# Optimization experiments

Measured on AMD Instinct MI355X. Metric: run time of the kernel, lower is better.

## Reference

```python
import jax, jax.numpy as jnp
import numpy as np

# Dims: N=batch graphs, V=grid nodes (128x128), D=feature dim, E=edges, L=gnn layers
N, V, D, E, L = 16, 16384, 128, 65536, 2
EPS = 1e-5  # BatchNorm1d default eps


def setup_inputs() -> dict:
    key = jax.random.key(0)
    ks = jax.random.split(key, 8)
    H = jax.random.normal(ks[0], (N, V, D), dtype=jnp.float32)
    edge_src = jax.random.randint(ks[1], (E,), 0, V, dtype=jnp.int32)
    edge_dst = jax.random.randint(ks[2], (E,), 0, V, dtype=jnp.int32)
    A_vals = jax.random.uniform(ks[3], (E,), dtype=jnp.float32)
    scale = 1.0 / np.sqrt(D).astype(np.float32)
    # Stacked per-layer params. Linear stores weight as [out, in]; y = x @ W.T
    W_self = jax.random.normal(ks[4], (L, D, D), dtype=jnp.float32) * scale
    W_nei = jax.random.normal(ks[5], (L, D, D), dtype=jnp.float32) * scale
    gamma = jnp.ones((L, D), dtype=jnp.float32)
    beta = jnp.zeros((L, D), dtype=jnp.float32)
    return {"H": H, "edge_src": edge_src, "edge_dst": edge_dst, "A_vals": A_vals,
            "W_self": W_self, "W_nei": W_nei, "gamma": gamma, "beta": beta}


def reference(H, edge_src, edge_dst, A_vals, W_self, W_nei, gamma, beta):
    X = H  # [N, V, D]
    for l in range(L):
        # SpMM: X_nei[n] = A_norm @ X[n], batched over N via vmap.
        msg = X[:, edge_src, :] * A_vals[None, :, None]  # [N, E, D]
        X_nei = jax.vmap(
            lambda m: jax.ops.segment_sum(m, edge_dst, num_segments=V)
        )(msg)  # [N, V, D]
        # y = x @ W.T for torch Linear(weight=[out,in])
        Y = (jnp.einsum('nvd,ed->nve', X, W_self[l])
             + jnp.einsum('nvd,ed->nve', X_nei, W_nei[l]))  # [N, V, D]
        # BatchNorm1d in training mode over the flattened (N*V) batch dim
        mean = jnp.mean(Y, axis=(0, 1))            # [D]
        var = jnp.var(Y, axis=(0, 1))              # biased variance, [D]
        Y = (Y - mean) * jax.lax.rsqrt(var + EPS) * gamma[l] + beta[l]
        X = jax.nn.relu(Y)
    return X
```

## Files before the change

kernel.cpp:

```cpp
#include <hip/hip_runtime.h>

#define N_ 16
#define V_ 16384
#define D_ 128
#define E_ 65536
#define L_ 2
#define M_ (N_*V_)


typedef __attribute__((ext_vector_type(8))) short short8;
typedef __attribute__((ext_vector_type(4))) float floatx4;

__device__ inline unsigned short f2bf(float x){
  unsigned u = __builtin_bit_cast(unsigned, x);
  unsigned r = u + 0x7fffu + ((u >> 16) & 1u);
  return (unsigned short)(r >> 16);
}
__device__ inline float bf2f(unsigned short h){
  unsigned u = ((unsigned)h) << 16;
  return __builtin_bit_cast(float, u);
}
__device__ inline unsigned pack2(float a, float b){
  return (unsigned)f2bf(a) | ((unsigned)f2bf(b) << 16);
}

__global__ __launch_bounds__(256) void conv_in_k(const float* __restrict__ H,
                                                 unsigned short* __restrict__ Xb){
  int v = blockIdx.x;
  int t = threadIdx.x;
  int n = t >> 4, dc = t & 15;
  const float4* h4 = (const float4*)H;
  size_t base = ((size_t)n * V_ + v) * 32 + (size_t)dc * 2;
  float4 a = h4[base], b = h4[base + 1];
  uint4 o;
  o.x = pack2(a.x, a.y);
  o.y = pack2(a.z, a.w);
  o.z = pack2(b.x, b.y);
  o.w = pack2(b.z, b.w);
  ((uint4*)Xb)[(size_t)v * 256 + t] = o;
}

__global__ __launch_bounds__(256) void conv_w_k(const float* __restrict__ Wself,
                                                const float* __restrict__ Wnei,
                                                unsigned short* __restrict__ Wb){
  int f = blockIdx.x * 256 + threadIdx.x;
  int lane = f & 63;
  int ct   = (f >> 6) & 7;
  int ks   = (f >> 9) & 3;
  int mat  = (f >> 11) & 1;
  int l    = (f >> 12) & 1;
  int e = ct * 16 + (lane & 15);
  int d = ks * 32 + (lane >> 4) * 8;
  const float* src = (mat ? Wnei : Wself) + ((size_t)l * D_ * D_ + e * D_ + d);
  uint4 o;
  o.x = pack2(src[0], src[1]);
  o.y = pack2(src[2], src[3]);
  o.z = pack2(src[4], src[5]);
  o.w = pack2(src[6], src[7]);
  ((uint4*)Wb)[f] = o;
}

__global__ __launch_bounds__(256) void hist_k(const int* __restrict__ dst, int* __restrict__ cnt){
  int e = blockIdx.x * 256 + threadIdx.x;
  atomicAdd(&cnt[dst[e]], 1);
}

__global__ __launch_bounds__(256) void scan_k(const int* __restrict__ cnt, int* __restrict__ row_ptr){
  __shared__ int part[256];
  int t = threadIdx.x;
  int base = t * 64;
  int s = 0;
  for (int i = 0; i < 64; ++i) s += cnt[base + i];
  part[t] = s;
  __syncthreads();
  for (int d = 1; d < 256; d <<= 1){
    int v = (t >= d) ? part[t - d] : 0;
    __syncthreads();
    part[t] += v;
    __syncthreads();
  }
  int off = part[t] - s;
  for (int i = 0; i < 64; ++i){
    row_ptr[base + i] = off;
    off += cnt[base + i];
  }
  if (t == 255) row_ptr[V_] = off;
}

__global__ __launch_bounds__(256) void scatter_k(const int* __restrict__ src,
                                                 const int* __restrict__ dst,
                                                 const float* __restrict__ vals,
                                                 const int* __restrict__ row_ptr,
                                                 int* __restrict__ fill,
                                                 int* __restrict__ csr_col,
                                                 float* __restrict__ csr_val){
  int e = blockIdx.x * 256 + threadIdx.x;
  int d = dst[e];
  int pos = row_ptr[d] + atomicAdd(&fill[d], 1);
  csr_col[pos] = src[e];
  csr_val[pos] = vals[e];
}

template<int NORM>
__global__ __launch_bounds__(256) void spmm_k(const uint4* __restrict__ X,
                                              const int* __restrict__ row_ptr,
                                              const int* __restrict__ csr_col,
                                              const float* __restrict__ csr_val,
                                              const float* __restrict__ scsh,
                                              uint4* __restrict__ Xnei){
  int v = blockIdx.x;
  int t = threadIdx.x;
  float4 sc0 = {0,0,0,0}, sc1 = {0,0,0,0}, sh0 = {0,0,0,0}, sh1 = {0,0,0,0};
  if (NORM){
    int d0 = (t & 15) * 8;
    sc0 = *(const float4*)(scsh + d0);
    sc1 = *(const float4*)(scsh + d0 + 4);
    sh0 = *(const float4*)(scsh + 128 + d0);
    sh1 = *(const float4*)(scsh + 128 + d0 + 4);
  }
  int r0 = row_ptr[v], r1 = row_ptr[v + 1];
  float acc[8] = {0.f,0.f,0.f,0.f,0.f,0.f,0.f,0.f};
  for (int i = r0; i < r1; ++i){
    int c = csr_col[i];
    float a = csr_val[i];
    uint4 w = X[(size_t)c * 256 + t];
    float x[8];
    x[0] = bf2f((unsigned short)(w.x & 0xffff)); x[1] = bf2f((unsigned short)(w.x >> 16));
    x[2] = bf2f((unsigned short)(w.y & 0xffff)); x[3] = bf2f((unsigned short)(w.y >> 16));
    x[4] = bf2f((unsigned short)(w.z & 0xffff)); x[5] = bf2f((unsigned short)(w.z >> 16));
    x[6] = bf2f((unsigned short)(w.w & 0xffff)); x[7] = bf2f((unsigned short)(w.w >> 16));
    if (NORM){
      x[0] = fmaxf(0.f, x[0] * sc0.x + sh0.x);
      x[1] = fmaxf(0.f, x[1] * sc0.y + sh0.y);
      x[2] = fmaxf(0.f, x[2] * sc0.z + sh0.z);
      x[3] = fmaxf(0.f, x[3] * sc0.w + sh0.w);
      x[4] = fmaxf(0.f, x[4] * sc1.x + sh1.x);
      x[5] = fmaxf(0.f, x[5] * sc1.y + sh1.y);
      x[6] = fmaxf(0.f, x[6] * sc1.z + sh1.z);
      x[7] = fmaxf(0.f, x[7] * sc1.w + sh1.w);
    }
#pragma unroll
    for (int j = 0; j < 8; ++j) acc[j] += a * x[j];
  }
  uint4 o;
  o.x = pack2(acc[0], acc[1]);
  o.y = pack2(acc[2], acc[3]);
  o.z = pack2(acc[4], acc[5]);
  o.w = pack2(acc[6], acc[7]);
  Xnei[(size_t)v * 256 + t] = o;
}

template<int NORM>
__global__ __launch_bounds__(256, 2) void gemm_k(const unsigned short* __restrict__ Xs,
                                                 const unsigned short* __restrict__ Xn,
                                                 const uint4* __restrict__ Wfrag,
                                                 const float* __restrict__ scsh,
                                                 unsigned short* __restrict__ Yb,
                                                 float* __restrict__ stats){
  __shared__ uint4 lds_w[4096];
  __shared__ float lds_s[256];
  int tid = threadIdx.x;
  for (int i = tid; i < 4096; i += 256) lds_w[i] = Wfrag[i];
  if (NORM) lds_s[tid] = scsh[tid];
  __syncthreads();

  int wave = tid >> 6, lane = tid & 63;
  int quad = lane >> 4, l15 = lane & 15;
  int row0 = blockIdx.x * 128 + wave * 32;

  floatx4 zero = {0.f, 0.f, 0.f, 0.f};
  floatx4 acc[2][8];
#pragma unroll
  for (int rt = 0; rt < 2; ++rt)
#pragma unroll
    for (int ct = 0; ct < 8; ++ct) acc[rt][ct] = zero;

  const short8* lw = (const short8*)lds_w;
#pragma unroll
  for (int ks = 0; ks < 4; ++ks){
    float scv[8], shv[8];
    if (NORM){
      int cb = ks * 32 + quad * 8;
#pragma unroll
      for (int j = 0; j < 8; ++j){
        scv[j] = lds_s[cb + j];
        shv[j] = lds_s[128 + cb + j];
      }
    }
    short8 a_s[2], a_n[2];
#pragma unroll
    for (int rt = 0; rt < 2; ++rt){
      size_t r = (size_t)(row0 + rt * 16 + l15);
      short8 raw = *(const short8*)(Xs + r * 128 + ks * 32 + quad * 8);
      if (NORM){
        short8 t;
#pragma unroll
        for (int j = 0; j < 8; ++j){
          float x = bf2f((unsigned short)raw[j]);
          x = fmaxf(0.f, x * scv[j] + shv[j]);
          t[j] = (short)f2bf(x);
        }
        a_s[rt] = t;
      } else {
        a_s[rt] = raw;
      }
      a_n[rt] = *(const short8*)(Xn + r * 128 + ks * 32 + quad * 8);
    }
#pragma unroll
    for (int ct = 0; ct < 8; ++ct){
      short8 bs = lw[((0 * 4 + ks) * 8 + ct) * 64 + lane];
      short8 bn = lw[((1 * 4 + ks) * 8 + ct) * 64 + lane];
#pragma unroll
      for (int rt = 0; rt < 2; ++rt){
        acc[rt][ct] = __builtin_amdgcn_mfma_f32_16x16x32_bf16(a_s[rt], bs, acc[rt][ct], 0, 0, 0);
        acc[rt][ct] = __builtin_amdgcn_mfma_f32_16x16x32_bf16(a_n[rt], bn, acc[rt][ct], 0, 0, 0);
      }
    }
  }

  float* sum_base = stats;
  float* sq_base  = stats + 64 * 128;
  int slot = blockIdx.x & 63;
#pragma unroll
  for (int rt = 0; rt < 2; ++rt){
    int rowq = row0 + rt * 16 + quad * 4;
#pragma unroll
    for (int ct = 0; ct < 8; ++ct){
      int col = ct * 16 + l15;
      float s = 0.f, q = 0.f;
#pragma unroll
      for (int rg = 0; rg < 4; ++rg){
        float yv = acc[rt][ct][rg];
        Yb[(size_t)(rowq + rg) * 128 + col] = f2bf(yv);
        s += yv; q += yv * yv;
      }
      s += __shfl_xor(s, 16); s += __shfl_xor(s, 32);
      q += __shfl_xor(q, 16); q += __shfl_xor(q, 32);
      if (lane < 16)      atomicAdd(&sum_base[slot * 128 + ct * 16 + lane], s);
      else if (lane < 32) atomicAdd(&sq_base [slot * 128 + ct * 16 + (lane & 15)], q);
    }
  }
}

__global__ __launch_bounds__(128) void finalize_k(const float* __restrict__ stats,
                                                  const float* __restrict__ gamma,
                                                  const float* __restrict__ beta,
                                                  float* __restrict__ scsh){
  int d = threadIdx.x;
  float s = 0.f, q = 0.f;
  for (int k = 0; k < 64; ++k){
    s += stats[k * 128 + d];
    q += stats[64 * 128 + k * 128 + d];
  }
  float inv = 1.0f / (float)M_;
  float mean = s * inv;
  float var  = q * inv - mean * mean;
  float rstd = rsqrtf(var + 1e-5f);
  float scale = gamma[d] * rstd;
  scsh[d]       = scale;
  scsh[128 + d] = beta[d] - mean * scale;
}

__global__ __launch_bounds__(256) void bn_out_k(const uint4* __restrict__ Y,
                                                const float* __restrict__ scsh,
                                                float4* __restrict__ out){
  int v = blockIdx.x;
  int t = threadIdx.x;
  int n = t >> 4, dc = t & 15;
  uint4 y = Y[(size_t)v * 256 + t];
  int d0 = dc * 8;
  float4 sc0 = *(const float4*)(scsh + d0);
  float4 sc1 = *(const float4*)(scsh + d0 + 4);
  float4 sh0 = *(const float4*)(scsh + 128 + d0);
  float4 sh1 = *(const float4*)(scsh + 128 + d0 + 4);
  float4 o0, o1;
  o0.x = fmaxf(0.f, bf2f((unsigned short)(y.x & 0xffff)) * sc0.x + sh0.x);
  o0.y = fmaxf(0.f, bf2f((unsigned short)(y.x >> 16))    * sc0.y + sh0.y);
  o0.z = fmaxf(0.f, bf2f((unsigned short)(y.y & 0xffff)) * sc0.z + sh0.z);
  o0.w = fmaxf(0.f, bf2f((unsigned short)(y.y >> 16))    * sc0.w + sh0.w);
  o1.x = fmaxf(0.f, bf2f((unsigned short)(y.z & 0xffff)) * sc1.x + sh1.x);
  o1.y = fmaxf(0.f, bf2f((unsigned short)(y.z >> 16))    * sc1.y + sh1.y);
  o1.z = fmaxf(0.f, bf2f((unsigned short)(y.w & 0xffff)) * sc1.z + sh1.z);
  o1.w = fmaxf(0.f, bf2f((unsigned short)(y.w >> 16))    * sc1.w + sh1.w);
  size_t ob = ((size_t)n * V_ + v) * 32 + (size_t)dc * 2;
  out[ob]     = o0;
  out[ob + 1] = o1;
}

static inline size_t align_up(size_t x, size_t a){ return (x + a - 1) & ~(a - 1); }

extern "C" void kernel_launch(void* const* d_in, const int* in_sizes, int n_in,
                              void* d_out, int out_size, void* d_ws, size_t ws_size,
                              hipStream_t stream){
  const float* H     = (const float*)d_in[0];
  const int*   esrc  = (const int*)  d_in[1];
  const int*   edst  = (const int*)  d_in[2];
  const float* avals = (const float*)d_in[3];
  const float* Wself = (const float*)d_in[4];
  const float* Wnei  = (const float*)d_in[5];
  const float* gamma = (const float*)d_in[6];
  const float* beta  = (const float*)d_in[7];

  char* ws = (char*)d_ws;
  size_t off = 0;
  unsigned short* Xb   = (unsigned short*)(ws + off); off += align_up((size_t)M_ * D_ * 2, 256);
  unsigned short* Xnei = (unsigned short*)(ws + off); off += align_up((size_t)M_ * D_ * 2, 256);
  unsigned short* Y0   = (unsigned short*)(ws + off); off += align_up((size_t)M_ * D_ * 2, 256);
  unsigned short* Wb   = (unsigned short*)(ws + off); off += align_up((size_t)L_ * 2 * D_ * D_ * 2, 256);
  int*   row_ptr = (int*)  (ws + off); off += align_up((size_t)(V_ + 1) * 4, 256);
  int*   csr_col = (int*)  (ws + off); off += align_up((size_t)E_ * 4, 256);
  float* csr_val = (float*)(ws + off); off += align_up((size_t)E_ * 4, 256);
  float* scsh0   = (float*)(ws + off); off += align_up((size_t)2 * 128 * 4, 256);
  float* scsh1   = (float*)(ws + off); off += align_up((size_t)2 * 128 * 4, 256);
  char* zbase = ws + off;
  int*   cnt    = (int*)  (ws + off); off += (size_t)V_ * 4;
  int*   fill   = (int*)  (ws + off); off += (size_t)V_ * 4;
  float* stats0 = (float*)(ws + off); off += (size_t)64 * 128 * 2 * 4;
  float* stats1 = (float*)(ws + off); off += (size_t)64 * 128 * 2 * 4;
  size_t zbytes = (size_t)(ws + off - zbase);
  unsigned short* Y1 = Xb;
  (void)ws_size; (void)in_sizes; (void)n_in; (void)out_size;

  conv_in_k<<<V_, 256, 0, stream>>>(H, Xb);
  conv_w_k<<<8192 / 256, 256, 0, stream>>>(Wself, Wnei, Wb);
  hipMemsetAsync(zbase, 0, zbytes, stream);
  hist_k<<<E_ / 256, 256, 0, stream>>>(edst, cnt);
  scan_k<<<1, 256, 0, stream>>>(cnt, row_ptr);
  scatter_k<<<E_ / 256, 256, 0, stream>>>(esrc, edst, avals, row_ptr, fill, csr_col, csr_val);

  spmm_k<0><<<V_, 256, 0, stream>>>((const uint4*)Xb, row_ptr, csr_col, csr_val,
                                    nullptr, (uint4*)Xnei);
  gemm_k<0><<<M_ / 128, 256, 0, stream>>>(Xb, Xnei, (const uint4*)Wb, nullptr, Y0, stats0);
  finalize_k<<<1, 128, 0, stream>>>(stats0, gamma, beta, scsh0);

  spmm_k<1><<<V_, 256, 0, stream>>>((const uint4*)Y0, row_ptr, csr_col, csr_val,
                                    scsh0, (uint4*)Xnei);
  gemm_k<1><<<M_ / 128, 256, 0, stream>>>(Y0, Xnei, (const uint4*)Wb + 4096, scsh0, Y1, stats1);
  finalize_k<<<1, 128, 0, stream>>>(stats1, gamma + 128, beta + 128, scsh1);
  bn_out_k<<<V_, 256, 0, stream>>>((const uint4*)Y1, scsh1, (float4*)d_out);
}
```

Baseline: 505.8 us.

## Fuse SpMM neighbor aggregation into GEMM kernel and reduce BN stats in LDS

Removes the separate SpMM kernel. Each GEMM wave now gathers and accumulates the neighbor rows for its two graph nodes in registers, converts them to bf16 and feeds them straight to the MFMA, so the intermediate Xnei buffer is never written to or read back from global memory. Per-column BatchNorm sum and sum-of-squares are first combined across waves in LDS, leaving one atomic per column per block. The cost is a serial, latency-bound gather loop inside the GEMM that walks the edge list once per k-slice, plus higher register pressure.

```diff
diff --git a/kernel.cpp b/kernel.cpp
--- a/kernel.cpp
+++ b/kernel.cpp
@@ -102,63 +102,17 @@
 }
 
 template<int NORM>
-__global__ __launch_bounds__(256) void spmm_k(const uint4* __restrict__ X,
-                                              const int* __restrict__ row_ptr,
-                                              const int* __restrict__ csr_col,
-                                              const float* __restrict__ csr_val,
-                                              const float* __restrict__ scsh,
-                                              uint4* __restrict__ Xnei){
-  int v = blockIdx.x;
-  int t = threadIdx.x;
-  float4 sc0 = {0,0,0,0}, sc1 = {0,0,0,0}, sh0 = {0,0,0,0}, sh1 = {0,0,0,0};
-  if (NORM){
-    int d0 = (t & 15) * 8;
-    sc0 = *(const float4*)(scsh + d0);
-    sc1 = *(const float4*)(scsh + d0 + 4);
-    sh0 = *(const float4*)(scsh + 128 + d0);
-    sh1 = *(const float4*)(scsh + 128 + d0 + 4);
-  }
-  int r0 = row_ptr[v], r1 = row_ptr[v + 1];
-  float acc[8] = {0.f,0.f,0.f,0.f,0.f,0.f,0.f,0.f};
-  for (int i = r0; i < r1; ++i){
-    int c = csr_col[i];
-    float a = csr_val[i];
-    uint4 w = X[(size_t)c * 256 + t];
-    float x[8];
-    x[0] = bf2f((unsigned short)(w.x & 0xffff)); x[1] = bf2f((unsigned short)(w.x >> 16));
-    x[2] = bf2f((unsigned short)(w.y & 0xffff)); x[3] = bf2f((unsigned short)(w.y >> 16));
-    x[4] = bf2f((unsigned short)(w.z & 0xffff)); x[5] = bf2f((unsigned short)(w.z >> 16));
-    x[6] = bf2f((unsigned short)(w.w & 0xffff)); x[7] = bf2f((unsigned short)(w.w >> 16));
-    if (NORM){
-      x[0] = fmaxf(0.f, x[0] * sc0.x + sh0.x);
-      x[1] = fmaxf(0.f, x[1] * sc0.y + sh0.y);
-      x[2] = fmaxf(0.f, x[2] * sc0.z + sh0.z);
-      x[3] = fmaxf(0.f, x[3] * sc0.w + sh0.w);
-      x[4] = fmaxf(0.f, x[4] * sc1.x + sh1.x);
-      x[5] = fmaxf(0.f, x[5] * sc1.y + sh1.y);
-      x[6] = fmaxf(0.f, x[6] * sc1.z + sh1.z);
-      x[7] = fmaxf(0.f, x[7] * sc1.w + sh1.w);
-    }
-#pragma unroll
-    for (int j = 0; j < 8; ++j) acc[j] += a * x[j];
-  }
-  uint4 o;
-  o.x = pack2(acc[0], acc[1]);
-  o.y = pack2(acc[2], acc[3]);
-  o.z = pack2(acc[4], acc[5]);
-  o.w = pack2(acc[6], acc[7]);
-  Xnei[(size_t)v * 256 + t] = o;
-}
-
-template<int NORM>
-__global__ __launch_bounds__(256, 2) void gemm_k(const unsigned short* __restrict__ Xs,
-                                                 const unsigned short* __restrict__ Xn,
+__global__ __launch_bounds__(256, 2) void gemm_k(const unsigned short* __restrict__ X,
                                                  const uint4* __restrict__ Wfrag,
                                                  const float* __restrict__ scsh,
+                                                 const int* __restrict__ row_ptr,
+                                                 const int* __restrict__ csr_col,
+                                                 const float* __restrict__ csr_val,
                                                  unsigned short* __restrict__ Yb,
                                                  float* __restrict__ stats){
   __shared__ uint4 lds_w[4096];
   __shared__ float lds_s[256];
+  __shared__ float lds_red[4 * 256];
   int tid = threadIdx.x;
   for (int i = tid; i < 4096; i += 256) lds_w[i] = Wfrag[i];
   if (NORM) lds_s[tid] = scsh[tid];
@@ -167,6 +121,51 @@
   int wave = tid >> 6, lane = tid & 63;
   int quad = lane >> 4, l15 = lane & 15;
   int row0 = blockIdx.x * 128 + wave * 32;
+  int v0 = row0 >> 4;
+
+  float accn[2][4][8];
+#pragma unroll
+  for (int rt = 0; rt < 2; ++rt)
+#pragma unroll
+    for (int ks = 0; ks < 4; ++ks)
+#pragma unroll
+      for (int j = 0; j < 8; ++j) accn[rt][ks][j] = 0.f;
+
+#pragma unroll
+  for (int rt = 0; rt < 2; ++rt){
+    int v = v0 + rt;
+    int r0 = row_ptr[v], r1 = row_ptr[v + 1];
+#pragma unroll
+    for (int ks = 0; ks < 4; ++ks){
+      float scv[8], shv[8];
+      if (NORM){
+        int cb = ks * 32 + quad * 8;
+#pragma unroll
+        for (int j = 0; j < 8; ++j){
+          scv[j] = lds_s[cb + j];
+          shv[j] = lds_s[128 + cb + j];
+        }
+      }
+      for (int i = r0; i < r1; ++i){
+        int c = csr_col[i];
+        float a = csr_val[i];
+        short8 w = *(const short8*)(X + ((size_t)c * 16 + l15) * 128 + ks * 32 + quad * 8);
+#pragma unroll
+        for (int j = 0; j < 8; ++j){
+          float x = bf2f((unsigned short)w[j]);
+          if (NORM) x = fmaxf(0.f, x * scv[j] + shv[j]);
+          accn[rt][ks][j] += a * x;
+        }
+      }
+    }
+  }
+  short8 a_n[2][4];
+#pragma unroll
+  for (int rt = 0; rt < 2; ++rt)
+#pragma unroll
+    for (int ks = 0; ks < 4; ++ks)
+#pragma unroll
+      for (int j = 0; j < 8; ++j) a_n[rt][ks][j] = (short)f2bf(accn[rt][ks][j]);
 
   floatx4 zero = {0.f, 0.f, 0.f, 0.f};
   floatx4 acc[2][8];
@@ -187,11 +186,11 @@
         shv[j] = lds_s[128 + cb + j];
       }
     }
-    short8 a_s[2], a_n[2];
+    short8 a_s[2];
 #pragma unroll
     for (int rt = 0; rt < 2; ++rt){
       size_t r = (size_t)(row0 + rt * 16 + l15);
-      short8 raw = *(const short8*)(Xs + r * 128 + ks * 32 + quad * 8);
+      short8 raw = *(const short8*)(X + r * 128 + ks * 32 + quad * 8);
       if (NORM){
         short8 t;
 #pragma unroll
@@ -204,7 +203,6 @@
       } else {
         a_s[rt] = raw;
       }
-      a_n[rt] = *(const short8*)(Xn + r * 128 + ks * 32 + quad * 8);
     }
 #pragma unroll
     for (int ct = 0; ct < 8; ++ct){
@@ -213,14 +211,12 @@
 #pragma unroll
       for (int rt = 0; rt < 2; ++rt){
         acc[rt][ct] = __builtin_amdgcn_mfma_f32_16x16x32_bf16(a_s[rt], bs, acc[rt][ct], 0, 0, 0);
-        acc[rt][ct] = __builtin_amdgcn_mfma_f32_16x16x32_bf16(a_n[rt], bn, acc[rt][ct], 0, 0, 0);
-      }
-    }
-  }
-
-  float* sum_base = stats;
-  float* sq_base  = stats + 64 * 128;
-  int slot = blockIdx.x & 63;
+        acc[rt][ct] = __builtin_amdgcn_mfma_f32_16x16x32_bf16(a_n[rt][ks], bn, acc[rt][ct], 0, 0, 0);
+      }
+    }
+  }
+
+  float* wred = lds_red + wave * 256;
 #pragma unroll
   for (int rt = 0; rt < 2; ++rt){
     int rowq = row0 + rt * 16 + quad * 4;
@@ -236,9 +232,22 @@
       }
       s += __shfl_xor(s, 16); s += __shfl_xor(s, 32);
       q += __shfl_xor(q, 16); q += __shfl_xor(q, 32);
-      if (lane < 16)      atomicAdd(&sum_base[slot * 128 + ct * 16 + lane], s);
-      else if (lane < 32) atomicAdd(&sq_base [slot * 128 + ct * 16 + (lane & 15)], q);
-    }
+      if (lane < 16){
+        if (rt == 0) wred[ct * 16 + lane] = s; else wred[ct * 16 + lane] += s;
+      } else if (lane < 32){
+        int c2 = ct * 16 + (lane & 15);
+        if (rt == 0) wred[128 + c2] = q; else wred[128 + c2] += q;
+      }
+    }
+  }
+  __syncthreads();
+  {
+    float tot = lds_red[tid] + lds_red[256 + tid] + lds_red[512 + tid] + lds_red[768 + tid];
+    int col = tid & 127;
+    int slot = blockIdx.x & 63;
+    float* dstp = (tid < 128) ? (stats + slot * 128 + col)
+                              : (stats + 64 * 128 + slot * 128 + col);
+    atomicAdd(dstp, tot);
   }
 }
 
@@ -304,7 +313,6 @@
   char* ws = (char*)d_ws;
   size_t off = 0;
   unsigned short* Xb   = (unsigned short*)(ws + off); off += align_up((size_t)M_ * D_ * 2, 256);
-  unsigned short* Xnei = (unsigned short*)(ws + off); off += align_up((size_t)M_ * D_ * 2, 256);
   unsigned short* Y0   = (unsigned short*)(ws + off); off += align_up((size_t)M_ * D_ * 2, 256);
   unsigned short* Wb   = (unsigned short*)(ws + off); off += align_up((size_t)L_ * 2 * D_ * D_ * 2, 256);
   int*   row_ptr = (int*)  (ws + off); off += align_up((size_t)(V_ + 1) * 4, 256);
@@ -328,14 +336,12 @@
   scan_k<<<1, 256, 0, stream>>>(cnt, row_ptr);
   scatter_k<<<E_ / 256, 256, 0, stream>>>(esrc, edst, avals, row_ptr, fill, csr_col, csr_val);
 
-  spmm_k<0><<<V_, 256, 0, stream>>>((const uint4*)Xb, row_ptr, csr_col, csr_val,
-                                    nullptr, (uint4*)Xnei);
-  gemm_k<0><<<M_ / 128, 256, 0, stream>>>(Xb, Xnei, (const uint4*)Wb, nullptr, Y0, stats0);
+  gemm_k<0><<<M_ / 128, 256, 0, stream>>>(Xb, (const uint4*)Wb, nullptr,
+                                          row_ptr, csr_col, csr_val, Y0, stats0);
   finalize_k<<<1, 128, 0, stream>>>(stats0, gamma, beta, scsh0);
 
-  spmm_k<1><<<V_, 256, 0, stream>>>((const uint4*)Y0, row_ptr, csr_col, csr_val,
-                                    scsh0, (uint4*)Xnei);
-  gemm_k<1><<<M_ / 128, 256, 0, stream>>>(Y0, Xnei, (const uint4*)Wb + 4096, scsh0, Y1, stats1);
+  gemm_k<1><<<M_ / 128, 256, 0, stream>>>(Y0, (const uint4*)Wb + 4096, scsh0,
+                                          row_ptr, csr_col, csr_val, Y1, stats1);
   finalize_k<<<1, 128, 0, stream>>>(stats1, gamma + 128, beta + 128, scsh1);
   bn_out_k<<<V_, 256, 0, stream>>>((const uint4*)Y1, scsh1, (float4*)d_out);
 }
```

After: 587.6 us. 1.16x slower.
